# Kernel optimization log

Measured on AMD Instinct MI355X. Metric: run time of the kernel, lower is better.

## Reference

```python
import jax, jax.numpy as jnp
import numpy as np


def setup_inputs() -> dict:
    key = jax.random.key(0)
    k1, k2 = jax.random.split(key)
    B, S, D = 4, 2048, 1024
    x = jax.random.normal(k1, (B, S, D), dtype=jnp.float32)
    # uniform initializer in keras is small; scale to keep softmax well-behaved
    kernel = jax.random.normal(k2, (3, D, D), dtype=jnp.float32) * 0.02
    return {"x": x, "kernel": kernel}


def reference(x, kernel):
    # x: [B, S, D], kernel: [3, D, D]
    D = x.shape[-1]
    q = jnp.einsum('bsd,de->bse', x, kernel[0])
    k = jnp.einsum('bsd,de->bse', x, kernel[1])
    v = jnp.einsum('bsd,de->bse', x, kernel[2])
    scores = jnp.einsum('bqe,bke->bqk', q, k) / jnp.sqrt(jnp.float32(D))
    attn = jax.nn.softmax(scores, axis=-1)
    return jnp.einsum('bqk,bke->bqe', attn, v)
```

## Files before the change

### kernel.cpp

```cpp
#include <hip/hip_runtime.h>
#include <hip/hip_bf16.h>
#include <cstdint>

typedef __bf16 bf16x8 __attribute__((ext_vector_type(8)));
typedef float f32x4 __attribute__((ext_vector_type(4)));

__device__ __forceinline__ unsigned short f2bf(float f) {
  union { float f; uint32_t u; } a; a.f = f;
  uint32_t r = a.u + 0x7fffu + ((a.u >> 16) & 1u);
  return (unsigned short)(r >> 16);
}
__device__ __forceinline__ void gload_lds16(const unsigned short* g, unsigned short* l) {
  __builtin_amdgcn_global_load_lds(
      (const __attribute__((address_space(1))) void*)g,
      (__attribute__((address_space(3))) void*)l, 16, 0, 0);
}

__global__ void cast_all(const float* __restrict__ x, const float* __restrict__ W,
                         unsigned short* __restrict__ xb, unsigned short* __restrict__ Wt) {
  __shared__ float tileW[64][65];
  const int bx = blockIdx.x;
  const int t = threadIdx.x;
  if (bx < 4096) {
    size_t i = ((size_t)bx * 256 + t) * 8;
    float4 a = *(const float4*)(x + i);
    float4 b = *(const float4*)(x + i + 4);
    uint4 o;
    o.x = (uint32_t)f2bf(a.x) | ((uint32_t)f2bf(a.y) << 16);
    o.y = (uint32_t)f2bf(a.z) | ((uint32_t)f2bf(a.w) << 16);
    o.z = (uint32_t)f2bf(b.x) | ((uint32_t)f2bf(b.y) << 16);
    o.w = (uint32_t)f2bf(b.z) | ((uint32_t)f2bf(b.w) << 16);
    *(uint4*)(xb + i) = o;
  } else {
    const int b = bx - 4096;
    const int z = b >> 8;
    const int rest = b & 255;
    const int bxx = rest & 15, byy = rest >> 4;
    const float* Wz = W + (size_t)z * 1048576;
    unsigned short* Wtz = Wt + (size_t)z * 1048576;
    const int x0 = bxx * 64, y0 = byy * 64;
    {
      const int r = t >> 4;
      const int c = (t & 15) * 4;
#pragma unroll
      for (int p = 0; p < 64; p += 16) {
        float4 v = *(const float4*)(Wz + (size_t)(y0 + p + r) * 1024 + x0 + c);
        tileW[p + r][c + 0] = v.x;
        tileW[p + r][c + 1] = v.y;
        tileW[p + r][c + 2] = v.z;
        tileW[p + r][c + 3] = v.w;
      }
    }
    __syncthreads();
    {
      const int dc = (t & 7) * 8;
#pragma unroll
      for (int p = 0; p < 64; p += 32) {
        const int e = p + (t >> 3);
        uint4 o;
        o.x = (uint32_t)f2bf(tileW[dc + 0][e]) | ((uint32_t)f2bf(tileW[dc + 1][e]) << 16);
        o.y = (uint32_t)f2bf(tileW[dc + 2][e]) | ((uint32_t)f2bf(tileW[dc + 3][e]) << 16);
        o.z = (uint32_t)f2bf(tileW[dc + 4][e]) | ((uint32_t)f2bf(tileW[dc + 5][e]) << 16);
        o.w = (uint32_t)f2bf(tileW[dc + 6][e]) | ((uint32_t)f2bf(tileW[dc + 7][e]) << 16);
        *(uint4*)(Wtz + (size_t)(x0 + e) * 1024 + y0 + dc) = o;
      }
    }
  }
}

__global__ void reduce_aux(const float* __restrict__ partial, float* __restrict__ rowinv) {
  const int r = blockIdx.x * 256 + threadIdx.x;
  float s = 0.f;
#pragma unroll
  for (int j = 0; j < 32; ++j) s += partial[(size_t)j * 8192 + r];
  rowinv[r] = 1.f / s;
}

template <int MODE>
__global__ void __launch_bounds__(256)
gemm_bt(const unsigned short* __restrict__ Aall,
        const unsigned short* __restrict__ Btall,
        void* __restrict__ Call, unsigned short* __restrict__ VtPtr,
        float* __restrict__ aux,
        int K, int ldc, long sA, long sB, long sC, float scale) {
  __shared__ unsigned short As[2][4096];
  __shared__ unsigned short Bs[2][4096];
  const int t = threadIdx.x;
  const int lane = t & 63;
  const int quad = lane >> 4;
  const int l15 = lane & 15;
  const int wave = t >> 6;
  const int wm = (wave >> 1) * 64;
  const int wn = (wave & 1) * 64;
  const int z = blockIdx.z;

  const unsigned short* A = Aall + (size_t)z * sA + (size_t)blockIdx.x * 128 * K;
  const unsigned short* Bt = Btall + (size_t)z * sB + (size_t)blockIdx.y * 128 * K;

  const int srow = t >> 2;
  const int scol = (((t & 3) ^ ((srow >> 1) & 3)) * 8);
  const unsigned short* ga = A + (size_t)srow * K + scol;
  const unsigned short* gb = Bt + (size_t)srow * K + scol;
  const size_t rowskip = (size_t)64 * K;

  const int aOff = (wm + l15) * 32 + (quad ^ ((l15 >> 1) & 3)) * 8;
  const int bOff = (wn + l15) * 32 + (quad ^ ((l15 >> 1) & 3)) * 8;

  f32x4 acc[4][4];
#pragma unroll
  for (int i = 0; i < 4; i++)
#pragma unroll
    for (int j = 0; j < 4; j++) acc[i][j] = (f32x4){0.f, 0.f, 0.f, 0.f};

  gload_lds16(ga, &As[0][t * 8]);
  gload_lds16(ga + rowskip, &As[0][2048 + t * 8]);
  gload_lds16(gb, &Bs[0][t * 8]);
  gload_lds16(gb + rowskip, &Bs[0][2048 + t * 8]);

  int buf = 0;
  for (int k0 = 0; k0 < K; k0 += 32, buf ^= 1) {
    __syncthreads();
    if (k0 + 32 < K) {
      const int kn = k0 + 32;
      gload_lds16(ga + kn, &As[buf ^ 1][t * 8]);
      gload_lds16(ga + rowskip + kn, &As[buf ^ 1][2048 + t * 8]);
      gload_lds16(gb + kn, &Bs[buf ^ 1][t * 8]);
      gload_lds16(gb + rowskip + kn, &Bs[buf ^ 1][2048 + t * 8]);
    }
    const unsigned short* aB = &As[buf][aOff];
    const unsigned short* bB = &Bs[buf][bOff];
    bf16x8 a[4], b[4];
#pragma unroll
    for (int i = 0; i < 4; i++) a[i] = *(const bf16x8*)(aB + i * 512);
#pragma unroll
    for (int j = 0; j < 4; j++) b[j] = *(const bf16x8*)(bB + j * 512);
#pragma unroll
    for (int i = 0; i < 4; i++)
#pragma unroll
      for (int j = 0; j < 4; j++)
        acc[i][j] = __builtin_amdgcn_mfma_f32_16x16x32_bf16(a[i], b[j], acc[i][j], 0, 0, 0);
  }

  const int mbase = blockIdx.x * 128 + wm + quad * 4;
  const int nbase = blockIdx.y * 128 + wn + l15;

  if (MODE == 4) {
    if (z < 2) {
      unsigned short* C = (unsigned short*)Call + (size_t)z * sC;
#pragma unroll
      for (int mi = 0; mi < 4; mi++)
#pragma unroll
        for (int ni = 0; ni < 4; ni++) {
          const int m = mbase + mi * 16, n = nbase + ni * 16;
#pragma unroll
          for (int r = 0; r < 4; r++)
            C[(size_t)(m + r) * ldc + n] = f2bf(acc[mi][ni][r]);
        }
    } else {
      unsigned short* C = VtPtr;
#pragma unroll
      for (int mi = 0; mi < 4; mi++) {
        const int m = mbase + mi * 16;
        const int b = m >> 11, s = m & 2047;
#pragma unroll
        for (int ni = 0; ni < 4; ni++) {
          const int n = nbase + ni * 16;
          uint2 val;
          val.x = (uint32_t)f2bf(acc[mi][ni][0]) | ((uint32_t)f2bf(acc[mi][ni][1]) << 16);
          val.y = (uint32_t)f2bf(acc[mi][ni][2]) | ((uint32_t)f2bf(acc[mi][ni][3]) << 16);
          *(uint2*)(C + (size_t)b * 2097152 + (size_t)n * 2048 + s) = val;
        }
      }
    }
  } else if (MODE == 5) {
    unsigned short* C = (unsigned short*)Call + (size_t)z * sC;
    const int j = blockIdx.y * 2 + (wn >> 6);
#pragma unroll
    for (int mi = 0; mi < 4; mi++) {
#pragma unroll
      for (int r = 0; r < 4; r++) {
        const int m = mbase + mi * 16 + r;
        float s = 0.f;
#pragma unroll
        for (int ni = 0; ni < 4; ni++) {
          const float e = __expf(acc[mi][ni][r] * scale);
          C[(size_t)m * ldc + nbase + ni * 16] = f2bf(e);
          s += e;
        }
        s += __shfl_xor(s, 1);
        s += __shfl_xor(s, 2);
        s += __shfl_xor(s, 4);
        s += __shfl_xor(s, 8);
        if (l15 == 0) aux[(size_t)j * 8192 + (size_t)z * 2048 + m] = s;
      }
    }
  } else {
    float* C = (float*)Call + (size_t)z * sC;
#pragma unroll
    for (int mi = 0; mi < 4; mi++) {
#pragma unroll
      for (int r = 0; r < 4; r++) {
        const int m = mbase + mi * 16 + r;
        const float inv = aux[(size_t)z * 2048 + m];
#pragma unroll
        for (int ni = 0; ni < 4; ni++)
          C[(size_t)m * ldc + nbase + ni * 16] = acc[mi][ni][r] * inv;
      }
    }
  }
}

extern "C" void kernel_launch(void* const* d_in, const int* in_sizes, int n_in,
                              void* d_out, int out_size, void* d_ws, size_t ws_size,
                              hipStream_t stream) {
  const float* x = (const float*)d_in[0];
  const float* W = (const float*)d_in[1];
  float* out = (float*)d_out;
  char* ws = (char*)d_ws;
  unsigned short* xb = (unsigned short*)(ws);
  unsigned short* Wt = (unsigned short*)(ws + (16ll << 20));
  float* partial     = (float*)(ws + (16ll << 20));
  float* rowinv      = (float*)(ws + (18ll << 20));
  unsigned short* Q  = (unsigned short*)(ws + (22ll << 20));
  unsigned short* Kb = (unsigned short*)(ws + (38ll << 20));
  unsigned short* Vt = (unsigned short*)(ws + (54ll << 20));
  unsigned short* Sb = (unsigned short*)(ws + (70ll << 20));

  cast_all<<<4864, 256, 0, stream>>>(x, W, xb, Wt);

  gemm_bt<4><<<dim3(64, 8, 3), 256, 0, stream>>>(
      xb, Wt, Q, Vt, nullptr, 1024, 1024, 0L, 1048576L, 8388608L, 1.0f);
  gemm_bt<5><<<dim3(16, 16, 4), 256, 0, stream>>>(
      Q, Kb, Sb, nullptr, partial, 1024, 2048, 2097152L, 2097152L, 4194304L, 0.03125f);
  reduce_aux<<<32, 256, 0, stream>>>(partial, rowinv);
  gemm_bt<6><<<dim3(16, 8, 4), 256, 0, stream>>>(
      Sb, Vt, out, nullptr, rowinv, 2048, 1024, 4194304L, 2097152L, 2097152L, 1.0f);
}
```

Baseline: 257.8 us.

## Deepen GEMM LDS pipeline to four stages with explicit vmcnt waits

The double-buffered K loop becomes a four-buffer pipeline that keeps three tiles of global-to-LDS loads in flight. Manual s_waitcnt vmcnt counts and a raw s_barrier replace __syncthreads, so each iteration waits only for the tile it is about to use. The goal is to hide more global memory latency behind the MFMA work. LDS use doubles to 64 KB per block, which may reduce occupancy, and correctness now depends on the hand-set vmcnt values matching the number of loads issued.

New measurement: 268.7 us. 1.04x slower.

```diff
diff --git a/kernel.cpp b/kernel.cpp
--- a/kernel.cpp
+++ b/kernel.cpp
@@ -83,8 +83,8 @@
         void* __restrict__ Call, unsigned short* __restrict__ VtPtr,
         float* __restrict__ aux,
         int K, int ldc, long sA, long sB, long sC, float scale) {
-  __shared__ unsigned short As[2][4096];
-  __shared__ unsigned short Bs[2][4096];
+  __shared__ unsigned short As[4][4096];
+  __shared__ unsigned short Bs[4][4096];
   const int t = threadIdx.x;
   const int lane = t & 63;
   const int quad = lane >> 4;
@@ -112,21 +112,31 @@
 #pragma unroll
     for (int j = 0; j < 4; j++) acc[i][j] = (f32x4){0.f, 0.f, 0.f, 0.f};
 
-  gload_lds16(ga, &As[0][t * 8]);
-  gload_lds16(ga + rowskip, &As[0][2048 + t * 8]);
-  gload_lds16(gb, &Bs[0][t * 8]);
-  gload_lds16(gb + rowskip, &Bs[0][2048 + t * 8]);
-
-  int buf = 0;
-  for (int k0 = 0; k0 < K; k0 += 32, buf ^= 1) {
-    __syncthreads();
-    if (k0 + 32 < K) {
-      const int kn = k0 + 32;
-      gload_lds16(ga + kn, &As[buf ^ 1][t * 8]);
-      gload_lds16(ga + rowskip + kn, &As[buf ^ 1][2048 + t * 8]);
-      gload_lds16(gb + kn, &Bs[buf ^ 1][t * 8]);
-      gload_lds16(gb + rowskip + kn, &Bs[buf ^ 1][2048 + t * 8]);
-    }
+  const int NT = K >> 5;
+
+#define STAGE(S) do {                                            \
+    const int kn_ = (S) * 32;                                    \
+    const int bf_ = (S) & 3;                                     \
+    gload_lds16(ga + kn_, &As[bf_][t * 8]);                      \
+    gload_lds16(ga + rowskip + kn_, &As[bf_][2048 + t * 8]);     \
+    gload_lds16(gb + kn_, &Bs[bf_][t * 8]);                      \
+    gload_lds16(gb + rowskip + kn_, &Bs[bf_][2048 + t * 8]);     \
+  } while (0)
+
+  STAGE(0);
+  if (NT > 1) STAGE(1);
+  if (NT > 2) STAGE(2);
+
+  for (int k = 0; k < NT; ++k) {
+    const int rem = NT - 1 - k;
+    if (rem >= 2)      asm volatile("s_waitcnt vmcnt(8)" ::: "memory");
+    else if (rem == 1) asm volatile("s_waitcnt vmcnt(4)" ::: "memory");
+    else               asm volatile("s_waitcnt vmcnt(0)" ::: "memory");
+    __builtin_amdgcn_s_barrier();
+    asm volatile("" ::: "memory");
+    if (k + 3 < NT) STAGE(k + 3);
+
+    const int buf = k & 3;
     const unsigned short* aB = &As[buf][aOff];
     const unsigned short* bB = &Bs[buf][bOff];
     bf16x8 a[4], b[4];
@@ -140,6 +150,7 @@
       for (int j = 0; j < 4; j++)
         acc[i][j] = __builtin_amdgcn_mfma_f32_16x16x32_bf16(a[i], b[j], acc[i][j], 0, 0, 0);
   }
+#undef STAGE
 
   const int mbase = blockIdx.x * 128 + wm + quad * 4;
   const int nbase = blockIdx.y * 128 + wn + l15;
```

## Replace scores GEMM with 256x256-tile, 8-wave, hand-pipelined kernel

Applied to the files above, without the earlier changes.

The QK^T scores GEMM with its fused exp and row-sum epilogue moves into a dedicated kernel. It uses 256x256 output tiles, 512 threads and 64-wide K steps split into two halves. The loop is explicitly staged, with interleaved async LDS loads, sched_barriers, setprio and manual vmcnt waits, so MFMA work overlaps with global-to-LDS transfers. The larger tile raises data reuse per LDS byte, at the cost of heavy LDS (128KB) and register pressure, and the grid shrinks to one block per CU.

Measured after the change: 241.9 us. -6.2%, faster.

```diff
diff --git a/kernel.cpp b/kernel.cpp
--- a/kernel.cpp
+++ b/kernel.cpp
@@ -82,7 +82,7 @@
         const unsigned short* __restrict__ Btall,
         void* __restrict__ Call, unsigned short* __restrict__ VtPtr,
         float* __restrict__ aux,
-        int K, int ldc, long sA, long sB, long sC, float scale) {
+        int K, int ldc, long sA, long sB, long sC) {
   __shared__ unsigned short As[2][4096];
   __shared__ unsigned short Bs[2][4096];
   const int t = threadIdx.x;
@@ -172,28 +172,6 @@
         }
       }
     }
-  } else if (MODE == 5) {
-    unsigned short* C = (unsigned short*)Call + (size_t)z * sC;
-    const int j = blockIdx.y * 2 + (wn >> 6);
-#pragma unroll
-    for (int mi = 0; mi < 4; mi++) {
-#pragma unroll
-      for (int r = 0; r < 4; r++) {
-        const int m = mbase + mi * 16 + r;
-        float s = 0.f;
-#pragma unroll
-        for (int ni = 0; ni < 4; ni++) {
-          const float e = __expf(acc[mi][ni][r] * scale);
-          C[(size_t)m * ldc + nbase + ni * 16] = f2bf(e);
-          s += e;
-        }
-        s += __shfl_xor(s, 1);
-        s += __shfl_xor(s, 2);
-        s += __shfl_xor(s, 4);
-        s += __shfl_xor(s, 8);
-        if (l15 == 0) aux[(size_t)j * 8192 + (size_t)z * 2048 + m] = s;
-      }
-    }
   } else {
     float* C = (float*)Call + (size_t)z * sC;
 #pragma unroll
@@ -206,6 +184,163 @@
         for (int ni = 0; ni < 4; ni++)
           C[(size_t)m * ldc + nbase + ni * 16] = acc[mi][ni][r] * inv;
       }
+    }
+  }
+}
+
+__global__ void __launch_bounds__(512, 2)
+gemm8_scores(const unsigned short* __restrict__ Aall,
+             const unsigned short* __restrict__ Btall,
+             unsigned short* __restrict__ Call, float* __restrict__ aux,
+             int K, int ldc, long sA, long sB, long sC, float scale) {
+  __shared__ unsigned short As[2][2][8192];
+  __shared__ unsigned short Bs[2][2][8192];
+  const int t = threadIdx.x;
+  const int lane = t & 63;
+  const int quad = lane >> 4;
+  const int l15 = lane & 15;
+  const int wave = t >> 6;
+  const int wm = wave >> 2;
+  const int wn = wave & 3;
+  const int z = blockIdx.z;
+  const int NT = K >> 6;
+
+  const unsigned short* Ab = Aall + (size_t)z * sA + (size_t)blockIdx.x * 256 * K;
+  const unsigned short* Bb = Btall + (size_t)z * sB + (size_t)blockIdx.y * 256 * K;
+
+  const int sc = (((t & 3) ^ ((t >> 3) & 3)) * 8);
+  const unsigned short* gA = Ab + (size_t)(t >> 2) * K + sc;
+  const unsigned short* gB = Bb + (size_t)(t >> 2) * K + sc;
+  const size_t half2 = (size_t)128 * K;
+
+  const int swz = (quad ^ ((l15 >> 1) & 3)) * 8;
+  const int aRd = (wm * 128 + l15) * 32 + swz;
+  const int bRd = (wn * 64 + l15) * 32 + swz;
+
+  f32x4 acc[8][4];
+#pragma unroll
+  for (int i = 0; i < 8; ++i)
+#pragma unroll
+    for (int j = 0; j < 4; ++j) acc[i][j] = (f32x4){0.f, 0.f, 0.f, 0.f};
+
+#define STG_A(TT, KH) do { \
+    const unsigned short* g_ = gA + (TT) * 64 + (KH) * 32; \
+    unsigned short* d_ = &As[(TT) & 1][KH][t * 8]; \
+    gload_lds16(g_, d_); \
+    gload_lds16(g_ + half2, d_ + 4096); \
+  } while (0)
+#define STG_B(TT, KH) do { \
+    const unsigned short* g_ = gB + (TT) * 64 + (KH) * 32; \
+    unsigned short* d_ = &Bs[(TT) & 1][KH][t * 8]; \
+    gload_lds16(g_, d_); \
+    gload_lds16(g_ + half2, d_ + 4096); \
+  } while (0)
+#define PHASE_OPEN() do { \
+    __builtin_amdgcn_sched_barrier(0); \
+    __builtin_amdgcn_s_barrier(); \
+    asm volatile("s_waitcnt lgkmcnt(0)" ::: "memory"); \
+    __builtin_amdgcn_sched_barrier(0); \
+    __builtin_amdgcn_s_setprio(1); \
+  } while (0)
+#define PHASE_CLOSE() do { \
+    __builtin_amdgcn_s_setprio(0); \
+    __builtin_amdgcn_sched_barrier(0); \
+    __builtin_amdgcn_s_barrier(); \
+  } while (0)
+
+  STG_B(0, 0); STG_A(0, 0); STG_B(0, 1); STG_A(0, 1);
+  STG_B(1, 0); STG_A(1, 0); STG_B(1, 1);
+  asm volatile("s_waitcnt vmcnt(6)" ::: "memory");
+  __builtin_amdgcn_s_barrier();
+
+  for (int kt = 0; kt < NT; ++kt) {
+    const int buf = kt & 1;
+    bf16x8 bb[4], a[4];
+
+#pragma unroll
+    for (int j = 0; j < 4; ++j) bb[j] = *(const bf16x8*)&Bs[buf][0][bRd + j * 512];
+#pragma unroll
+    for (int i = 0; i < 4; ++i) a[i] = *(const bf16x8*)&As[buf][0][aRd + i * 512];
+    if (kt + 1 < NT) STG_A(kt + 1, 1);
+    PHASE_OPEN();
+#pragma unroll
+    for (int i = 0; i < 4; ++i)
+#pragma unroll
+      for (int j = 0; j < 4; ++j)
+        acc[i][j] = __builtin_amdgcn_mfma_f32_16x16x32_bf16(a[i], bb[j], acc[i][j], 0, 0, 0);
+    PHASE_CLOSE();
+
+#pragma unroll
+    for (int i = 0; i < 4; ++i) a[i] = *(const bf16x8*)&As[buf][0][aRd + 2048 + i * 512];
+    if (kt + 2 < NT) STG_B(kt + 2, 0);
+    PHASE_OPEN();
+#pragma unroll
+    for (int i = 0; i < 4; ++i)
+#pragma unroll
+      for (int j = 0; j < 4; ++j)
+        acc[4 + i][j] = __builtin_amdgcn_mfma_f32_16x16x32_bf16(a[i], bb[j], acc[4 + i][j], 0, 0, 0);
+    PHASE_CLOSE();
+
+#pragma unroll
+    for (int j = 0; j < 4; ++j) bb[j] = *(const bf16x8*)&Bs[buf][1][bRd + j * 512];
+#pragma unroll
+    for (int i = 0; i < 4; ++i) a[i] = *(const bf16x8*)&As[buf][1][aRd + i * 512];
+    if (kt + 2 < NT) STG_A(kt + 2, 0);
+    PHASE_OPEN();
+#pragma unroll
+    for (int i = 0; i < 4; ++i)
+#pragma unroll
+      for (int j = 0; j < 4; ++j)
+        acc[i][j] = __builtin_amdgcn_mfma_f32_16x16x32_bf16(a[i], bb[j], acc[i][j], 0, 0, 0);
+    PHASE_CLOSE();
+
+#pragma unroll
+    for (int i = 0; i < 4; ++i) a[i] = *(const bf16x8*)&As[buf][1][aRd + 2048 + i * 512];
+    if (kt + 2 < NT) STG_B(kt + 2, 1);
+    __builtin_amdgcn_sched_barrier(0);
+    __builtin_amdgcn_s_barrier();
+    asm volatile("s_waitcnt lgkmcnt(0)" ::: "memory");
+    __builtin_amdgcn_sched_barrier(0);
+    __builtin_amdgcn_s_setprio(1);
+#pragma unroll
+    for (int i = 0; i < 4; ++i)
+#pragma unroll
+      for (int j = 0; j < 4; ++j)
+        acc[4 + i][j] = __builtin_amdgcn_mfma_f32_16x16x32_bf16(a[i], bb[j], acc[4 + i][j], 0, 0, 0);
+    __builtin_amdgcn_s_setprio(0);
+    __builtin_amdgcn_sched_barrier(0);
+    if (kt < NT - 2) {
+      asm volatile("s_waitcnt vmcnt(6)" ::: "memory");
+    } else if (kt == NT - 2) {
+      asm volatile("s_waitcnt vmcnt(0)" ::: "memory");
+    }
+    __builtin_amdgcn_s_barrier();
+  }
+#undef STG_A
+#undef STG_B
+#undef PHASE_OPEN
+#undef PHASE_CLOSE
+
+  const int mb = blockIdx.x * 256 + wm * 128 + quad * 4;
+  const int nb = blockIdx.y * 256 + wn * 64 + l15;
+  const int j = blockIdx.y * 4 + wn;
+#pragma unroll
+  for (int mi = 0; mi < 8; ++mi) {
+#pragma unroll
+    for (int r = 0; r < 4; ++r) {
+      const int m = mb + mi * 16 + r;
+      float s = 0.f;
+#pragma unroll
+      for (int ni = 0; ni < 4; ++ni) {
+        const float e = __expf(acc[mi][ni][r] * scale);
+        Call[(size_t)z * sC + (size_t)m * ldc + nb + ni * 16] = f2bf(e);
+        s += e;
+      }
+      s += __shfl_xor(s, 1);
+      s += __shfl_xor(s, 2);
+      s += __shfl_xor(s, 4);
+      s += __shfl_xor(s, 8);
+      if (l15 == 0) aux[(size_t)j * 8192 + (size_t)z * 2048 + m] = s;
     }
   }
 }
@@ -229,10 +364,10 @@
   cast_all<<<4864, 256, 0, stream>>>(x, W, xb, Wt);
 
   gemm_bt<4><<<dim3(64, 8, 3), 256, 0, stream>>>(
-      xb, Wt, Q, Vt, nullptr, 1024, 1024, 0L, 1048576L, 8388608L, 1.0f);
-  gemm_bt<5><<<dim3(16, 16, 4), 256, 0, stream>>>(
-      Q, Kb, Sb, nullptr, partial, 1024, 2048, 2097152L, 2097152L, 4194304L, 0.03125f);
+      xb, Wt, Q, Vt, nullptr, 1024, 1024, 0L, 1048576L, 8388608L);
+  gemm8_scores<<<dim3(8, 8, 4), 512, 0, stream>>>(
+      Q, Kb, Sb, partial, 1024, 2048, 2097152L, 2097152L, 4194304L, 0.03125f);
   reduce_aux<<<32, 256, 0, stream>>>(partial, rowinv);
   gemm_bt<6><<<dim3(16, 8, 4), 256, 0, stream>>>(
-      Sb, Vt, out, nullptr, rowinv, 2048, 1024, 4194304L, 2097152L, 2097152L, 1.0f);
-}
+      Sb, Vt, out, nullptr, rowinv, 2048, 1024, 4194304L, 2097152L, 2097152L);
+}
```
